# Kernel optimization log

Measured on AMD Instinct MI355X. Metric: run time of the kernel, lower is better.

The kernel has to match this reference:

```python
import jax, jax.numpy as jnp
import numpy as np

B, Q, K, D = 16, 2048, 2048, 512

def setup_inputs() -> dict:
    key = jax.random.key(0)
    k1, k2, k3 = jax.random.split(key, 3)
    query = jax.random.normal(k1, (B, Q, D), dtype=jnp.float32)
    values = jax.random.normal(k2, (B, K, D), dtype=jnp.float32)
    # nn.Linear(D, D, bias=False) weight, applied as values @ W.T
    W_attn = jax.random.normal(k3, (D, D), dtype=jnp.float32) * (1.0 / np.sqrt(D))
    return {"query": query, "values": values, "W_attn": W_attn}

def reference(query, values, W_attn):
    # keys = Linear(values) = values @ W_attn.T  -> [B, K, D]
    keys = jnp.einsum('bkd,ed->bke', values, W_attn)
    # scores[b,q,k] = query[b,q,:] . keys[b,k,:]
    scores = jnp.einsum('bqd,bkd->bqk', query, keys)
    attention_weights = jax.nn.softmax(scores, axis=-1)
    context = jnp.einsum('bqk,bkd->bqd', attention_weights, values)
    return (context, attention_weights)
```

## Files before the change

kernel.cpp:

```cpp
#include <hip/hip_runtime.h>
#include <hip/hip_bf16.h>


#define B_ 16
#define Q_ 2048
#define K_ 2048
#define D_ 512

typedef _Float16 half8  __attribute__((ext_vector_type(8)));
typedef _Float16 half4v __attribute__((ext_vector_type(4)));
typedef float    floatx4 __attribute__((ext_vector_type(4)));

__device__ __forceinline__ void gld16(const _Float16* g, _Float16* l) {
  __builtin_amdgcn_global_load_lds(
      (const __attribute__((address_space(1))) void*)g,
      (__attribute__((address_space(3))) void*)l, 16, 0, 0);
}

template <bool OUT_HALF>
__global__ __launch_bounds__(256, 2)
void gemm_bt_f16(const _Float16* __restrict__ A, const _Float16* __restrict__ Bm,
                 void* __restrict__ Cv, int M, int N, int Kd,
                 long sA, long sB, long sC)
{
  const int b  = blockIdx.z;
  const _Float16* Ab = A + (long)b * sA;
  const _Float16* Bb = Bm + (long)b * sB;
  const int m0 = blockIdx.y * 128, n0 = blockIdx.x * 128;

  __shared__ _Float16 As[128 * 32];
  __shared__ _Float16 Bs[128 * 32];

  const int tid = threadIdx.x, wave = tid >> 6, lane = tid & 63;
  const int wm = wave >> 1, wn = wave & 1;
  floatx4 acc[4][4] = {};

  const int srow = wave * 16 + (lane >> 2);
  const int skof = (lane & 3) * 8;
  _Float16* la0 = As + wave * 512 + lane * 8;
  _Float16* la1 = la0 + 2048;
  _Float16* lb0 = Bs + wave * 512 + lane * 8;
  _Float16* lb1 = lb0 + 2048;
  const _Float16* ga = Ab + (long)(m0 + srow) * Kd + skof;
  const _Float16* gb = Bb + (long)(n0 + srow) * Kd + skof;

  const int fr = lane & 15, fk = (lane >> 4) * 8;

  for (int k0 = 0; k0 < Kd; k0 += 32) {
    gld16(ga + k0, la0);
    gld16(ga + 64l * Kd + k0, la1);
    gld16(gb + k0, lb0);
    gld16(gb + 64l * Kd + k0, lb1);
    __syncthreads();

    half8 af[4], bf[4];
#pragma unroll
    for (int t = 0; t < 4; t++) {
      af[t] = *(const half8*)(As + (wm * 64 + t * 16 + fr) * 32 + fk);
      bf[t] = *(const half8*)(Bs + (wn * 64 + t * 16 + fr) * 32 + fk);
    }
#pragma unroll
    for (int mt = 0; mt < 4; mt++)
#pragma unroll
      for (int nt = 0; nt < 4; nt++)
        acc[mt][nt] = __builtin_amdgcn_mfma_f32_16x16x32_f16(af[mt], bf[nt], acc[mt][nt], 0, 0, 0);
    __syncthreads();
  }

  const int orow = (lane >> 4) * 4, ocol = lane & 15;
  if constexpr (OUT_HALF) {
    _Float16* Cp = (_Float16*)Cv + (long)b * sC;
#pragma unroll
    for (int mt = 0; mt < 4; mt++)
#pragma unroll
      for (int nt = 0; nt < 4; nt++)
#pragma unroll
        for (int r = 0; r < 4; r++)
          Cp[(long)(m0 + wm * 64 + mt * 16 + orow + r) * N + (n0 + wn * 64 + nt * 16 + ocol)] =
              (_Float16)acc[mt][nt][r];
  } else {
    float* Cp = (float*)Cv + (long)b * sC;
#pragma unroll
    for (int mt = 0; mt < 4; mt++)
#pragma unroll
      for (int nt = 0; nt < 4; nt++)
#pragma unroll
        for (int r = 0; r < 4; r++)
          Cp[(long)(m0 + wm * 64 + mt * 16 + orow + r) * N + (n0 + wn * 64 + nt * 16 + ocol)] =
              acc[mt][nt][r];
  }
}

template <bool OUT_HALF>
__global__ __launch_bounds__(256, 2)
void gemm_a32_bt(const float* __restrict__ A, const _Float16* __restrict__ Bm,
                 void* __restrict__ Cv, int M, int N, int Kd, int lda,
                 long sA, long sB, long sC)
{
  const int b  = blockIdx.z;
  const float*    Ab = A + (long)b * sA;
  const _Float16* Bb = Bm + (long)b * sB;
  const int m0 = blockIdx.y * 128, n0 = blockIdx.x * 128;

  __shared__ _Float16 As[128 * 32];
  __shared__ _Float16 Bs[128 * 32];

  const int tid = threadIdx.x, wave = tid >> 6, lane = tid & 63;
  const int wm = wave >> 1, wn = wave & 1;
  floatx4 acc[4][4] = {};

  const int srow = wave * 16 + (lane >> 2);
  const int skof = (lane & 3) * 8;
  _Float16* lb0 = Bs + wave * 512 + lane * 8;
  _Float16* lb1 = lb0 + 2048;
  const _Float16* gb = Bb + (long)(n0 + srow) * Kd + skof;

  const int arow = tid >> 1, akc = (tid & 1) * 16;
  const float* ga = Ab + (long)(m0 + arow) * lda + akc;

  const int fr = lane & 15, fk = (lane >> 4) * 8;

  for (int k0 = 0; k0 < Kd; k0 += 32) {
    gld16(gb + k0, lb0);
    gld16(gb + 64l * Kd + k0, lb1);

    const float* ap = ga + k0;
    float4 f0 = *(const float4*)(ap);
    float4 f1 = *(const float4*)(ap + 4);
    float4 f2 = *(const float4*)(ap + 8);
    float4 f3 = *(const float4*)(ap + 12);
    half8 h0, h1;
    h0[0] = (_Float16)f0.x; h0[1] = (_Float16)f0.y; h0[2] = (_Float16)f0.z; h0[3] = (_Float16)f0.w;
    h0[4] = (_Float16)f1.x; h0[5] = (_Float16)f1.y; h0[6] = (_Float16)f1.z; h0[7] = (_Float16)f1.w;
    h1[0] = (_Float16)f2.x; h1[1] = (_Float16)f2.y; h1[2] = (_Float16)f2.z; h1[3] = (_Float16)f2.w;
    h1[4] = (_Float16)f3.x; h1[5] = (_Float16)f3.y; h1[6] = (_Float16)f3.z; h1[7] = (_Float16)f3.w;
    *(half8*)(As + arow * 32 + akc)     = h0;
    *(half8*)(As + arow * 32 + akc + 8) = h1;

    __syncthreads();

    half8 af[4], bf[4];
#pragma unroll
    for (int t = 0; t < 4; t++) {
      af[t] = *(const half8*)(As + (wm * 64 + t * 16 + fr) * 32 + fk);
      bf[t] = *(const half8*)(Bs + (wn * 64 + t * 16 + fr) * 32 + fk);
    }
#pragma unroll
    for (int mt = 0; mt < 4; mt++)
#pragma unroll
      for (int nt = 0; nt < 4; nt++)
        acc[mt][nt] = __builtin_amdgcn_mfma_f32_16x16x32_f16(af[mt], bf[nt], acc[mt][nt], 0, 0, 0);
    __syncthreads();
  }

  const int orow = (lane >> 4) * 4, ocol = lane & 15;
  if constexpr (OUT_HALF) {
    _Float16* Cp = (_Float16*)Cv + (long)b * sC;
#pragma unroll
    for (int mt = 0; mt < 4; mt++)
#pragma unroll
      for (int nt = 0; nt < 4; nt++)
#pragma unroll
        for (int r = 0; r < 4; r++)
          Cp[(long)(m0 + wm * 64 + mt * 16 + orow + r) * N + (n0 + wn * 64 + nt * 16 + ocol)] =
              (_Float16)acc[mt][nt][r];
  } else {
    float* Cp = (float*)Cv + (long)b * sC;
#pragma unroll
    for (int mt = 0; mt < 4; mt++)
#pragma unroll
      for (int nt = 0; nt < 4; nt++)
#pragma unroll
        for (int r = 0; r < 4; r++)
          Cp[(long)(m0 + wm * 64 + mt * 16 + orow + r) * N + (n0 + wn * 64 + nt * 16 + ocol)] =
              acc[mt][nt][r];
  }
}

template <bool EMIT_H>
__global__ __launch_bounds__(256)
void softmax_rows(float* __restrict__ S, _Float16* __restrict__ P)
{
  float* p = S + (long)blockIdx.x * 2048;
  const int tid = threadIdx.x, lane = tid & 63, wave = tid >> 6;

  float4 v0 = *(const float4*)(p + tid * 4);
  float4 v1 = *(const float4*)(p + 1024 + tid * 4);

  float mx = fmaxf(fmaxf(fmaxf(v0.x, v0.y), fmaxf(v0.z, v0.w)),
                   fmaxf(fmaxf(v1.x, v1.y), fmaxf(v1.z, v1.w)));
#pragma unroll
  for (int off = 32; off; off >>= 1) mx = fmaxf(mx, __shfl_down(mx, off, 64));

  __shared__ float red[8];
  if (lane == 0) red[wave] = mx;
  __syncthreads();
  mx = fmaxf(fmaxf(red[0], red[1]), fmaxf(red[2], red[3]));

  v0.x = __expf(v0.x - mx); v0.y = __expf(v0.y - mx);
  v0.z = __expf(v0.z - mx); v0.w = __expf(v0.w - mx);
  v1.x = __expf(v1.x - mx); v1.y = __expf(v1.y - mx);
  v1.z = __expf(v1.z - mx); v1.w = __expf(v1.w - mx);

  float s = v0.x + v0.y + v0.z + v0.w + v1.x + v1.y + v1.z + v1.w;
#pragma unroll
  for (int off = 32; off; off >>= 1) s += __shfl_down(s, off, 64);
  if (lane == 0) red[4 + wave] = s;
  __syncthreads();
  s = red[4] + red[5] + red[6] + red[7];

  float inv = 1.0f / s;
  v0.x *= inv; v0.y *= inv; v0.z *= inv; v0.w *= inv;
  v1.x *= inv; v1.y *= inv; v1.z *= inv; v1.w *= inv;
  *(float4*)(p + tid * 4) = v0;
  *(float4*)(p + 1024 + tid * 4) = v1;

  if constexpr (EMIT_H) {
    _Float16* ph = P + (long)blockIdx.x * 2048;
    half4v h0, h1;
    h0[0] = (_Float16)v0.x; h0[1] = (_Float16)v0.y;
    h0[2] = (_Float16)v0.z; h0[3] = (_Float16)v0.w;
    h1[0] = (_Float16)v1.x; h1[1] = (_Float16)v1.y;
    h1[2] = (_Float16)v1.z; h1[3] = (_Float16)v1.w;
    *(half4v*)(ph + tid * 4) = h0;
    *(half4v*)(ph + 1024 + tid * 4) = h1;
  }
}

__global__ __launch_bounds__(256)
void convert_q(const float4* __restrict__ q, half4v* __restrict__ qh)
{
  long i = (long)blockIdx.x * 256 + threadIdx.x;
  float4 a = q[i];
  half4v h;
  h[0] = (_Float16)a.x; h[1] = (_Float16)a.y; h[2] = (_Float16)a.z; h[3] = (_Float16)a.w;
  qh[i] = h;
}

__global__ __launch_bounds__(256)
void transpose_v(const float* __restrict__ v, _Float16* __restrict__ vt)
{
  __shared__ float tile[32][33];
  const int b = blockIdx.z, kk = blockIdx.y * 32, ee = blockIdx.x * 32;
  const float* vp = v + (long)b * K_ * D_;
  _Float16* vtp = vt + (long)b * D_ * K_;
  const int tx = threadIdx.x & 31, ty = threadIdx.x >> 5;
#pragma unroll
  for (int i = 0; i < 32; i += 8)
    tile[ty + i][tx] = vp[(long)(kk + ty + i) * D_ + ee + tx];
  __syncthreads();
#pragma unroll
  for (int i = 0; i < 32; i += 8)
    vtp[(long)(ee + ty + i) * K_ + kk + tx] = (_Float16)tile[tx][ty + i];
}

extern "C" void kernel_launch(void* const* d_in, const int* in_sizes, int n_in,
                              void* d_out, int out_size, void* d_ws, size_t ws_size,
                              hipStream_t stream)
{
  const float* q = (const float*)d_in[0];
  const float* v = (const float*)d_in[1];
  const float* w = (const float*)d_in[2];

  float* ctx    = (float*)d_out;
  float* scores = ctx + (long)B_ * Q_ * D_;

  const long nQD = (long)B_ * Q_ * D_;
  const long nKD = (long)B_ * K_ * D_;
  const long nDK = (long)B_ * D_ * K_;
  const long nQK = (long)B_ * Q_ * K_;

  const size_t need_fast = (size_t)(512 * 512 + nDK + nQK) * sizeof(_Float16);
  const bool fast = ws_size >= need_fast;

  _Float16 *wh, *vth, *qh, *kh, *ph;
  if (fast) {
    wh  = (_Float16*)d_ws;
    vth = wh + 512 * 512;
    ph  = vth + nDK;
    qh  = ph;
    kh  = qh + nQD;
  } else {
    qh  = (_Float16*)d_ws;
    kh  = qh + nQD;
    vth = kh + nKD;
    wh  = vth + nDK;
    ph  = nullptr;
  }

  convert_q<<<16384, 256, 0, stream>>>((const float4*)q, (half4v*)qh);
  convert_q<<<256,   256, 0, stream>>>((const float4*)w, (half4v*)wh);
  transpose_v<<<dim3(D_ / 32, K_ / 32, B_), 256, 0, stream>>>(v, vth);

  gemm_a32_bt<true><<<dim3(D_ / 128, K_ / 128, B_), 256, 0, stream>>>(
      v, wh, kh, K_, D_, D_, D_, (long)K_ * D_, 0l, (long)K_ * D_);

  gemm_bt_f16<false><<<dim3(K_ / 128, Q_ / 128, B_), 256, 0, stream>>>(
      qh, kh, scores, Q_, K_, D_, (long)Q_ * D_, (long)K_ * D_, (long)Q_ * K_);

  if (fast)
    softmax_rows<true><<<B_ * Q_, 256, 0, stream>>>(scores, ph);
  else
    softmax_rows<false><<<B_ * Q_, 256, 0, stream>>>(scores, nullptr);

  if (fast)
    gemm_bt_f16<false><<<dim3(D_ / 128, Q_ / 128, B_), 256, 0, stream>>>(
        ph, vth, ctx, Q_, D_, K_, (long)Q_ * K_, (long)D_ * K_, (long)Q_ * D_);
  else
    gemm_a32_bt<false><<<dim3(D_ / 128, Q_ / 128, B_), 256, 0, stream>>>(
        scores, vth, ctx, Q_, D_, K_, K_, (long)Q_ * K_, (long)D_ * K_, (long)Q_ * D_);
}
```

Measured before the change: 788.9 us.

## Fuse QK^T scores GEMM with online softmax and in-kernel query conversion

```diff
diff --git a/kernel.cpp b/kernel.cpp
--- a/kernel.cpp
+++ b/kernel.cpp
@@ -15,6 +15,135 @@
   __builtin_amdgcn_global_load_lds(
       (const __attribute__((address_space(1))) void*)g,
       (__attribute__((address_space(3))) void*)l, 16, 0, 0);
+}
+
+__global__ __launch_bounds__(256, 2)
+void scores_softmax(const float* __restrict__ q, const _Float16* __restrict__ kh,
+                    float* __restrict__ scores, _Float16* __restrict__ ph)
+{
+  const int b = blockIdx.y, q0 = blockIdx.x * 64;
+  const float*    qb = q  + ((long)b * Q_ + q0) * D_;
+  const _Float16* kb = kh + (long)b * K_ * D_;
+  float*    Sb = scores + ((long)b * Q_ + q0) * (long)K_;
+  _Float16* Pb = ph     + ((long)b * Q_ + q0) * (long)K_;
+
+  __shared__ _Float16 Qs[16 * 64 * 32];
+  __shared__ _Float16 Bs[128 * 32];
+  __shared__ float rmax[2][64], rsum[2][64], rowm[64], rowl[64], rowscale[64];
+
+  const int tid = threadIdx.x, wave = tid >> 6, lane = tid & 63;
+  const int wm = wave >> 1, wn = wave & 1;
+
+  {
+    const int row = tid >> 2, cbase = (tid & 3) * 128;
+    const float* qr = qb + (long)row * D_ + cbase;
+#pragma unroll
+    for (int i = 0; i < 16; i++) {
+      float4 f0 = *(const float4*)(qr + i * 8);
+      float4 f1 = *(const float4*)(qr + i * 8 + 4);
+      half8 h;
+      h[0] = (_Float16)f0.x; h[1] = (_Float16)f0.y; h[2] = (_Float16)f0.z; h[3] = (_Float16)f0.w;
+      h[4] = (_Float16)f1.x; h[5] = (_Float16)f1.y; h[6] = (_Float16)f1.z; h[7] = (_Float16)f1.w;
+      const int kq = cbase + i * 8;
+      *(half8*)(Qs + (kq >> 5) * 2048 + row * 32 + (kq & 31)) = h;
+    }
+  }
+  if (tid < 64) { rowm[tid] = -1e30f; rowl[tid] = 0.f; }
+  __syncthreads();
+
+  const int srow = wave * 16 + (lane >> 2), skof = (lane & 3) * 8;
+  _Float16* lb0 = Bs + wave * 512 + lane * 8;
+  _Float16* lb1 = lb0 + 2048;
+  const int fr = lane & 15, fk = (lane >> 4) * 8;
+  const int orow = (lane >> 4) * 4, ocol = lane & 15;
+
+  for (int c2 = 0; c2 < 16; c2++) {
+    const int kc = c2 * 128;
+    floatx4 acc[2][4] = {};
+    const _Float16* gb = kb + (long)(kc + srow) * D_ + skof;
+
+    for (int k0 = 0; k0 < 512; k0 += 32) {
+      gld16(gb + k0, lb0);
+      gld16(gb + 64l * D_ + k0, lb1);
+      __syncthreads();
+      half8 af[2], bf[4];
+      const _Float16* qc = Qs + (k0 >> 5) * 2048;
+      af[0] = *(const half8*)(qc + (wm * 32 +  0 + fr) * 32 + fk);
+      af[1] = *(const half8*)(qc + (wm * 32 + 16 + fr) * 32 + fk);
+#pragma unroll
+      for (int nt = 0; nt < 4; nt++)
+        bf[nt] = *(const half8*)(Bs + (wn * 64 + nt * 16 + fr) * 32 + fk);
+#pragma unroll
+      for (int mt = 0; mt < 2; mt++)
+#pragma unroll
+        for (int nt = 0; nt < 4; nt++)
+          acc[mt][nt] = __builtin_amdgcn_mfma_f32_16x16x32_f16(af[mt], bf[nt], acc[mt][nt], 0, 0, 0);
+      __syncthreads();
+    }
+
+#pragma unroll
+    for (int mt = 0; mt < 2; mt++) {
+#pragma unroll
+      for (int r = 0; r < 4; r++) {
+        const int row = wm * 32 + mt * 16 + orow + r;
+        float vm = -1e30f;
+#pragma unroll
+        for (int nt = 0; nt < 4; nt++) {
+          const float sv = acc[mt][nt][r];
+          Sb[(long)row * K_ + (kc + wn * 64 + nt * 16 + ocol)] = sv;
+          vm = fmaxf(vm, sv);
+        }
+#pragma unroll
+        for (int d = 1; d < 16; d <<= 1) vm = fmaxf(vm, __shfl_xor(vm, d, 64));
+        if ((lane & 15) == 0) rmax[wn][row] = vm;
+      }
+    }
+    __syncthreads();
+    if (tid < 64) {
+      const float cm = fmaxf(rmax[0][tid], rmax[1][tid]);
+      const float mo = rowm[tid];
+      const float mn = fmaxf(mo, cm);
+      rowm[tid] = mn;
+      rowscale[tid] = __expf(mo - mn);
+    }
+    __syncthreads();
+#pragma unroll
+    for (int mt = 0; mt < 2; mt++) {
+#pragma unroll
+      for (int r = 0; r < 4; r++) {
+        const int row = wm * 32 + mt * 16 + orow + r;
+        const float mn = rowm[row];
+        float sm = 0.f;
+#pragma unroll
+        for (int nt = 0; nt < 4; nt++) sm += __expf(acc[mt][nt][r] - mn);
+#pragma unroll
+        for (int d = 1; d < 16; d <<= 1) sm += __shfl_xor(sm, d, 64);
+        if ((lane & 15) == 0) rsum[wn][row] = sm;
+      }
+    }
+    __syncthreads();
+    if (tid < 64) rowl[tid] = rowl[tid] * rowscale[tid] + rsum[0][tid] + rsum[1][tid];
+    __syncthreads();
+  }
+
+  for (int r = 0; r < 64; r++) {
+    const float m = rowm[r];
+    const float invl = 1.0f / rowl[r];
+    float*    sp = Sb + (long)r * K_ + tid * 8;
+    _Float16* pp = Pb + (long)r * K_ + tid * 8;
+    float4 f0 = *(const float4*)sp;
+    float4 f1 = *(const float4*)(sp + 4);
+    f0.x = __expf(f0.x - m) * invl; f0.y = __expf(f0.y - m) * invl;
+    f0.z = __expf(f0.z - m) * invl; f0.w = __expf(f0.w - m) * invl;
+    f1.x = __expf(f1.x - m) * invl; f1.y = __expf(f1.y - m) * invl;
+    f1.z = __expf(f1.z - m) * invl; f1.w = __expf(f1.w - m) * invl;
+    *(float4*)sp = f0;
+    *(float4*)(sp + 4) = f1;
+    half8 h;
+    h[0] = (_Float16)f0.x; h[1] = (_Float16)f0.y; h[2] = (_Float16)f0.z; h[3] = (_Float16)f0.w;
+    h[4] = (_Float16)f1.x; h[5] = (_Float16)f1.y; h[6] = (_Float16)f1.z; h[7] = (_Float16)f1.w;
+    *(half8*)pp = h;
+  }
 }
 
 template <bool OUT_HALF>
@@ -115,8 +244,9 @@
   _Float16* lb1 = lb0 + 2048;
   const _Float16* gb = Bb + (long)(n0 + srow) * Kd + skof;
 
-  const int arow = tid >> 1, akc = (tid & 1) * 16;
-  const float* ga = Ab + (long)(m0 + arow) * lda + akc;
+  const int arow = tid >> 1;
+  const int akc  = ((tid & 1) * 16) ^ ((arow & 1) << 4);
+  const float* ga = Ab + (long)(m0 + arow) * lda + (tid & 1) * 16;
 
   const int fr = lane & 15, fk = (lane >> 4) * 8;
 
@@ -142,7 +272,8 @@
     half8 af[4], bf[4];
 #pragma unroll
     for (int t = 0; t < 4; t++) {
-      af[t] = *(const half8*)(As + (wm * 64 + t * 16 + fr) * 32 + fk);
+      const int ra = wm * 64 + t * 16 + fr;
+      af[t] = *(const half8*)(As + ra * 32 + (fk ^ ((ra & 1) << 4)));
       bf[t] = *(const half8*)(Bs + (wn * 64 + t * 16 + fr) * 32 + fk);
     }
 #pragma unroll
@@ -270,43 +401,44 @@
   const long nDK = (long)B_ * D_ * K_;
   const long nQK = (long)B_ * Q_ * K_;
 
-  const size_t need_fast = (size_t)(512 * 512 + nDK + nQK) * sizeof(_Float16);
+  const size_t need_fast = (size_t)(512 * 512 + nDK + nKD + nQK) * sizeof(_Float16);
   const bool fast = ws_size >= need_fast;
 
-  _Float16 *wh, *vth, *qh, *kh, *ph;
   if (fast) {
-    wh  = (_Float16*)d_ws;
-    vth = wh + 512 * 512;
-    ph  = vth + nDK;
-    qh  = ph;
-    kh  = qh + nQD;
-  } else {
-    qh  = (_Float16*)d_ws;
-    kh  = qh + nQD;
-    vth = kh + nKD;
-    wh  = vth + nDK;
-    ph  = nullptr;
-  }
-
-  convert_q<<<16384, 256, 0, stream>>>((const float4*)q, (half4v*)qh);
-  convert_q<<<256,   256, 0, stream>>>((const float4*)w, (half4v*)wh);
-  transpose_v<<<dim3(D_ / 32, K_ / 32, B_), 256, 0, stream>>>(v, vth);
-
-  gemm_a32_bt<true><<<dim3(D_ / 128, K_ / 128, B_), 256, 0, stream>>>(
-      v, wh, kh, K_, D_, D_, D_, (long)K_ * D_, 0l, (long)K_ * D_);
-
-  gemm_bt_f16<false><<<dim3(K_ / 128, Q_ / 128, B_), 256, 0, stream>>>(
-      qh, kh, scores, Q_, K_, D_, (long)Q_ * D_, (long)K_ * D_, (long)Q_ * K_);
-
-  if (fast)
-    softmax_rows<true><<<B_ * Q_, 256, 0, stream>>>(scores, ph);
-  else
-    softmax_rows<false><<<B_ * Q_, 256, 0, stream>>>(scores, nullptr);
-
-  if (fast)
+    _Float16* wh  = (_Float16*)d_ws;
+    _Float16* vth = wh + 512 * 512;
+    _Float16* kh  = vth + nDK;
+    _Float16* ph  = kh + nKD;
+
+    convert_q<<<256, 256, 0, stream>>>((const float4*)w, (half4v*)wh);
+    transpose_v<<<dim3(D_ / 32, K_ / 32, B_), 256, 0, stream>>>(v, vth);
+
+    gemm_a32_bt<true><<<dim3(D_ / 128, K_ / 128, B_), 256, 0, stream>>>(
+        v, wh, kh, K_, D_, D_, D_, (long)K_ * D_, 0l, (long)K_ * D_);
+
+    scores_softmax<<<dim3(Q_ / 64, B_), 256, 0, stream>>>(q, kh, scores, ph);
+
     gemm_bt_f16<false><<<dim3(D_ / 128, Q_ / 128, B_), 256, 0, stream>>>(
         ph, vth, ctx, Q_, D_, K_, (long)Q_ * K_, (long)D_ * K_, (long)Q_ * D_);
-  else
+  } else {
+    _Float16* qh  = (_Float16*)d_ws;
+    _Float16* kh  = qh + nQD;
+    _Float16* vth = kh + nKD;
+    _Float16* wh  = vth + nDK;
+
+    convert_q<<<16384, 256, 0, stream>>>((const float4*)q, (half4v*)qh);
+    convert_q<<<256,   256, 0, stream>>>((const float4*)w, (half4v*)wh);
+    transpose_v<<<dim3(D_ / 32, K_ / 32, B_), 256, 0, stream>>>(v, vth);
+
+    gemm_a32_bt<true><<<dim3(D_ / 128, K_ / 128, B_), 256, 0, stream>>>(
+        v, wh, kh, K_, D_, D_, D_, (long)K_ * D_, 0l, (long)K_ * D_);
+
+    gemm_bt_f16<false><<<dim3(K_ / 128, Q_ / 128, B_), 256, 0, stream>>>(
+        qh, kh, scores, Q_, K_, D_, (long)Q_ * D_, (long)K_ * D_, (long)Q_ * K_);
+
+    softmax_rows<false><<<B_ * Q_, 256, 0, stream>>>(scores, nullptr);
+
     gemm_a32_bt<false><<<dim3(D_ / 128, Q_ / 128, B_), 256, 0, stream>>>(
         scores, vth, ctx, Q_, D_, K_, K_, (long)Q_ * K_, (long)D_ * K_, (long)Q_ * D_);
-}
+  }
+}
```

Result: slower. 867.5 us (+10.0%).
